# Optimization experiments

Measured on AMD Instinct MI355X. Metric: run time of the kernel, lower is better.

## Reference

```python
import jax, jax.numpy as jnp
import numpy as np

N, E, FE = 20000, 160000, 500000
IN, HC, HEADS = 128, 64, 4
HEADC = HC // HEADS          # 16
DV = HEADC                   # 16
KHOP = 3
NUM_T = 128
OUT = 1
CST = 1e-5


def _lin(key, fan_in, fan_out):
    kw, kb = jax.random.split(key)
    s = 1.0 / np.sqrt(fan_in)
    W = jax.random.uniform(kw, (fan_in, fan_out), minval=-s, maxval=s, dtype=jnp.float32)
    b = jax.random.uniform(kb, (fan_out,), minval=-s, maxval=s, dtype=jnp.float32)
    return W, b


def setup_inputs() -> dict:
    key = jax.random.key(0)
    ks = jax.random.split(key, 16)
    x = jax.random.normal(ks[0], (N, IN), dtype=jnp.float32)
    edge_index = jax.random.randint(ks[1], (2, E), 0, N, dtype=jnp.int32)
    full_edge_index = jax.random.randint(ks[2], (2, FE), 0, N, dtype=jnp.int32)
    time_steps = jax.random.randint(ks[3], (N,), 0, NUM_T, dtype=jnp.int32)
    Wi, bi = _lin(ks[4], IN, HC)
    Wt1, bt1 = _lin(ks[5], HC, 4 * HC)
    Wt2, bt2 = _lin(ks[6], 4 * HC, HC)
    WQ, bQ = _lin(ks[7], HC, HEADS * HEADC)
    WK, bK = _lin(ks[8], HC, HEADS * HEADC)
    WV, bV = _lin(ks[9], HC, HEADS * DV)
    Wo, bo = _lin(ks[10], HEADS * DV, DV)
    hopwise = jnp.ones((KHOP + 1,), dtype=jnp.float32)
    headwise = jnp.zeros((HEADS, KHOP), dtype=jnp.float32)
    Wf1, bf1 = _lin(ks[11], 2 * DV, DV)
    Wf2, bf2 = _lin(ks[12], DV, OUT)
    return dict(x=x, edge_index=edge_index, full_edge_index=full_edge_index,
                time_steps=time_steps, Wi=Wi, bi=bi, Wt1=Wt1, bt1=bt1,
                Wt2=Wt2, bt2=bt2, WQ=WQ, bQ=bQ, WK=WK, bK=bK, WV=WV, bV=bV,
                Wo=Wo, bo=bo, hopwise=hopwise, headwise=headwise,
                Wf1=Wf1, bf1=bf1, Wf2=Wf2, bf2=bf2)


def _sin_emb(t, dim, num_steps, rescale=4000.0):
    # Sinusoidal timestep embedding rescaled by num_steps (diffusion style).
    t = t.astype(jnp.float32) * (rescale / num_steps)
    half = dim // 2
    freqs = jnp.exp(-jnp.log(10000.0) / (half - 1) * jnp.arange(half, dtype=jnp.float32))
    args = t[:, None] * freqs[None, :]
    return jnp.concatenate([jnp.sin(args), jnp.cos(args)], axis=-1)


def reference(x, edge_index, full_edge_index, time_steps,
              Wi, bi, Wt1, bt1, Wt2, bt2, WQ, bQ, WK, bK, WV, bV,
              Wo, bo, hopwise, headwise, Wf1, bf1, Wf2, bf2):
    n = x.shape[0]
    row, col = edge_index[0], edge_index[1]

    # random-walk norm: deg over destination (col), norm gathered at source (row)
    deg = jax.ops.segment_sum(jnp.ones_like(col, dtype=x.dtype), col, num_segments=n)
    deg_inv = jnp.where(deg > 0, 1.0 / deg, 0.0)
    norm = deg_inv[row]                                   # [E]

    t_emb = _sin_emb(time_steps, HC, NUM_T)               # [N, HC]
    t_emb = jax.nn.silu(t_emb @ Wt1 + bt1) @ Wt2 + bt2    # [N, HC]

    h = jax.nn.relu(x @ Wi + bi + t_emb)                  # [N, HC]

    Q = (1.0 + jax.nn.elu(h @ WQ + bQ)).reshape(n, HEADS, HEADC)
    Kf = (1.0 + jax.nn.elu(h @ WK + bK)).reshape(n, HEADS, HEADC)
    V = (h @ WV + bV).reshape(n, HEADS, DV)

    M = jnp.einsum('nhi,nhj->nhij', Kf, V)                # [N, H, hc, dv]
    hidden = V * hopwise[0]
    layerwise = jax.nn.softmax(headwise, axis=0)          # softmax over heads

    for hop in range(KHOP):
        # gather-scale-scatter message passing (random walk propagation)
        M = jax.ops.segment_sum(M[row] * norm[:, None, None, None], col, num_segments=n)
        Kf = jax.ops.segment_sum(Kf[row] * norm[:, None, None], col, num_segments=n)
        H = jnp.einsum('nhi,nhij->nhj', Q, M)             # [N, H, dv]
        C = jnp.einsum('nhi,nhi->nh', Q, Kf)[..., None] + CST
        gamma = hopwise[hop + 1] * layerwise[:, hop][:, None]   # [H, 1]
        hidden = hidden + gamma * (H / C)

    # multi_concat output projection
    hidden = hidden.reshape(n, HEADS * DV) @ Wo + bo      # [N, DV]

    src, dst = full_edge_index[0], full_edge_index[1]
    he = jnp.concatenate([hidden[src], hidden[dst]], axis=-1)  # [FE, 2*DV]
    edge_logits = jax.nn.silu(he @ Wf1 + bf1) @ Wf2 + bf2      # [FE, OUT]
    return edge_logits, hidden
```

## Files before the change

kernel.cpp:

```cpp
#include <hip/hip_runtime.h>
#include <math.h>


#define HC 64
#define HEADS 4
#define KHOP 3
#define NUM_T 128
#define MSZ 1024
#define SLOTS 64
#define CST 1e-5f

typedef float f32x2 __attribute__((ext_vector_type(2)));

__device__ __forceinline__ float bf2f(unsigned short s) { return __uint_as_float(((unsigned int)s) << 16); }
__device__ __forceinline__ float bfu_lo(unsigned int u) { return __uint_as_float(u << 16); }
__device__ __forceinline__ float bfu_hi(unsigned int u) { return __uint_as_float(u & 0xffff0000u); }
__device__ __forceinline__ unsigned short f2bf(float f) {
    unsigned int u = __float_as_uint(f);
    u = (u + 0x7fffu + ((u >> 16) & 1u)) >> 16;
    return (unsigned short)u;
}
__device__ __forceinline__ unsigned int pack4fp8(float a, float b, float c, float d) {
    int r = __builtin_amdgcn_cvt_pk_fp8_f32(a, b, 0, false);
    r = __builtin_amdgcn_cvt_pk_fp8_f32(c, d, r, true);
    return (unsigned int)r;
}

__global__ void k_fill(const int* __restrict__ row, const int* __restrict__ col,
                       int* __restrict__ cnt, int* __restrict__ csr, int E) {
    int e = blockIdx.x * 256 + threadIdx.x;
    if (e >= E) return;
    int c = col[e];
    int r = row[e];
    int k = atomicAdd(&cnt[c], 1);
    if (k < SLOTS) csr[c * SLOTS + k] = r;
}

__global__ __launch_bounds__(256) void k_misc(
    const float* __restrict__ Wt1, const float* __restrict__ bt1,
    const float* __restrict__ Wt2, const float* __restrict__ bt2,
    const float* __restrict__ hopwise, const float* __restrict__ headwise,
    const int* __restrict__ cnt,
    float* __restrict__ gamma, float* __restrict__ table,
    float* __restrict__ inv_deg, int n) {
    if (blockIdx.x >= 32) {
        int i = (blockIdx.x - 32) * 256 + threadIdx.x;
        if (i < n) {
            int d = cnt[i];
            inv_deg[i] = (d > 0) ? 1.0f / (float)min(d, SLOTS) : 0.0f;
        }
        return;
    }
    if (blockIdx.x == 0 && threadIdx.x == 0) {
        for (int k = 0; k < KHOP; k++) {
            float m = -1e30f;
            for (int h2 = 0; h2 < HEADS; h2++) m = fmaxf(m, headwise[h2 * KHOP + k]);
            float ex[HEADS]; float s = 0.f;
            for (int h2 = 0; h2 < HEADS; h2++) { ex[h2] = expf(headwise[h2 * KHOP + k] - m); s += ex[h2]; }
            for (int h2 = 0; h2 < HEADS; h2++) gamma[k * HEADS + h2] = hopwise[k + 1] * ex[h2] / s;
        }
    }
    int slot = threadIdx.x >> 6;
    int j = threadIdx.x & 63;
    int tval = blockIdx.x * 4 + slot;
    __shared__ float emb_s[4][64];
    __shared__ float z1_s[4][256];
    {
        float t = (float)tval * 31.25f;
        float e;
        if (j < 32) e = sinf(t * expf(-0.2971077539347156f * (float)j));
        else        e = cosf(t * expf(-0.2971077539347156f * (float)(j - 32)));
        emb_s[slot][j] = e;
    }
    __syncthreads();
    {
        #pragma unroll
        for (int k = 0; k < 4; k++) {
            int o = j + 64 * k;
            float acc = bt1[o];
            for (int i = 0; i < 64; i++) acc += emb_s[slot][i] * Wt1[i * 256 + o];
            z1_s[slot][o] = acc / (1.f + expf(-acc));
        }
    }
    __syncthreads();
    {
        float acc = bt2[j];
        for (int i = 0; i < 256; i++) acc += z1_s[slot][i] * Wt2[i * 64 + j];
        table[tval * 64 + j] = acc;
    }
}

__global__ __launch_bounds__(256) void k_node(
    const float* __restrict__ x, const int* __restrict__ time_steps,
    const float* __restrict__ temb, const float* __restrict__ Wi,
    const float* __restrict__ bi,
    const float* __restrict__ WQ, const float* __restrict__ bQ,
    const float* __restrict__ WK, const float* __restrict__ bK,
    const float* __restrict__ WV, const float* __restrict__ bV,
    const float* __restrict__ hopwise, const float* __restrict__ inv_deg,
    float* __restrict__ Q, unsigned short* __restrict__ Kf0,
    unsigned short* __restrict__ Vbuf, float* __restrict__ hidden, int n) {
    __shared__ float xs[16][128];
    __shared__ float hs[16][64];
    int j = threadIdx.x & 63;
    int slot = threadIdx.x >> 6;
    int nbase = blockIdx.x * 16;
    int nvalid = min(16, n - nbase);
    const float4* xg = (const float4*)(x + (size_t)nbase * 128);
    float4* xs4 = (float4*)&xs[0][0];
    for (int idx = threadIdx.x; idx < nvalid * 32; idx += 256) xs4[idx] = xg[idx];
    __syncthreads();
    int nl = slot * 4;
    {
        float acc[4];
        #pragma unroll
        for (int k = 0; k < 4; k++) acc[k] = 0.f;
        #pragma unroll 8
        for (int i = 0; i < 128; i++) {
            float w = Wi[i * 64 + j];
            #pragma unroll
            for (int k = 0; k < 4; k++) acc[k] += xs[nl + k][i] * w;
        }
        float bj = bi[j];
        #pragma unroll
        for (int k = 0; k < 4; k++) {
            int node = nbase + nl + k;
            float te = (node < n) ? temb[time_steps[node] * 64 + j] : 0.f;
            hs[nl + k][j] = fmaxf(acc[k] + bj + te, 0.f);
        }
    }
    __syncthreads();
    float aq[4], ak[4], av[4];
    #pragma unroll
    for (int k = 0; k < 4; k++) { aq[k] = bQ[j]; ak[k] = bK[j]; av[k] = bV[j]; }
    #pragma unroll 4
    for (int i = 0; i < 64; i++) {
        float wq = WQ[i * 64 + j], wk = WK[i * 64 + j], wv = WV[i * 64 + j];
        #pragma unroll
        for (int k = 0; k < 4; k++) {
            float hv = hs[nl + k][i];
            aq[k] += hv * wq; ak[k] += hv * wk; av[k] += hv * wv;
        }
    }
    float h0 = hopwise[0];
    #pragma unroll
    for (int k = 0; k < 4; k++) {
        int node = nbase + nl + k;
        if (node < n) {
            float q  = 1.f + ((aq[k] > 0.f) ? aq[k] : (expf(aq[k]) - 1.f));
            float kf = 1.f + ((ak[k] > 0.f) ? ak[k] : (expf(ak[k]) - 1.f));
            float inv = inv_deg[node];
            Q[(size_t)node * 64 + j] = q;
            Kf0[(size_t)node * 64 + j] = f2bf(kf * inv);
            Vbuf[(size_t)node * 64 + j] = f2bf(av[k]);
            hidden[(size_t)node * 64 + j] = av[k] * h0;
        }
    }
}

template<int MODE>
__global__ __launch_bounds__(256) void k_hop(
    const unsigned char* __restrict__ Mold, const unsigned short* __restrict__ Kfold,
    const unsigned short* __restrict__ Vbuf,
    const int* __restrict__ cnt, const int* __restrict__ csr,
    const float* __restrict__ inv_deg, const float* __restrict__ Q,
    const float* __restrict__ gamma,
    unsigned char* __restrict__ Mnew, unsigned short* __restrict__ Kfnew,
    float* __restrict__ hidden, int hop, int write_out,
    const float* __restrict__ Wo, const float* __restrict__ bo,
    const float* __restrict__ Wf1, float* __restrict__ out16,
    float* __restrict__ Pbuf, int n) {
    constexpr int DEPTH = (MODE == 0) ? 4 : 8;
    int lane = threadIdx.x & 63;
    int node = blockIdx.x * 4 + (threadIdx.x >> 6);
    if (node >= n) return;
    int grp = lane >> 4;
    int deg = min(cnt[node], SLOTS);
    int degU = __builtin_amdgcn_readfirstlane(deg);
    int sidx = csr[(size_t)node * SLOTS + lane];
    float qv = Q[(size_t)node * 64 + lane];
    float acc[16];
    #pragma unroll
    for (int t = 0; t < 16; t++) acc[t] = 0.f;
    float kacc = 0.f;

    for (int base = 0; base < degU; base += DEPTH) {
        unsigned short kraw[DEPTH];
        uint4 m0[DEPTH], m1[DEPTH];
        #pragma unroll
        for (int t = 0; t < DEPTH; t++) {
            int d = base + t;
            int dc = (d < degU) ? d : (degU - 1);
            int s = __builtin_amdgcn_readlane(sidx, dc);
            kraw[t] = Kfold[(size_t)s * 64 + lane];
            if constexpr (MODE == 0) {
                const uint4* vp = (const uint4*)((const unsigned char*)Vbuf + (size_t)s * 128 + grp * 32);
                m0[t] = vp[0];
                m1[t] = vp[1];
            } else {
                m0[t] = *(const uint4*)(Mold + (size_t)s * MSZ + lane * 16);
            }
        }
        #pragma unroll
        for (int t = 0; t < DEPTH; t++) {
            float wt = (base + t < degU) ? 1.f : 0.f;
            float kf = bf2f(kraw[t]);
            kacc = fmaf(wt, kf, kacc);
            if constexpr (MODE == 0) {
                float kw = kf * wt;
                acc[0]  = fmaf(kw, bfu_lo(m0[t].x), acc[0]);
                acc[1]  = fmaf(kw, bfu_hi(m0[t].x), acc[1]);
                acc[2]  = fmaf(kw, bfu_lo(m0[t].y), acc[2]);
                acc[3]  = fmaf(kw, bfu_hi(m0[t].y), acc[3]);
                acc[4]  = fmaf(kw, bfu_lo(m0[t].z), acc[4]);
                acc[5]  = fmaf(kw, bfu_hi(m0[t].z), acc[5]);
                acc[6]  = fmaf(kw, bfu_lo(m0[t].w), acc[6]);
                acc[7]  = fmaf(kw, bfu_hi(m0[t].w), acc[7]);
                acc[8]  = fmaf(kw, bfu_lo(m1[t].x), acc[8]);
                acc[9]  = fmaf(kw, bfu_hi(m1[t].x), acc[9]);
                acc[10] = fmaf(kw, bfu_lo(m1[t].y), acc[10]);
                acc[11] = fmaf(kw, bfu_hi(m1[t].y), acc[11]);
                acc[12] = fmaf(kw, bfu_lo(m1[t].z), acc[12]);
                acc[13] = fmaf(kw, bfu_hi(m1[t].z), acc[13]);
                acc[14] = fmaf(kw, bfu_lo(m1[t].w), acc[14]);
                acc[15] = fmaf(kw, bfu_hi(m1[t].w), acc[15]);
            } else {
                f32x2 p;
                p = __builtin_amdgcn_cvt_pk_f32_fp8((int)m0[t].x, false); acc[0]  = fmaf(wt, p.x, acc[0]);  acc[1]  = fmaf(wt, p.y, acc[1]);
                p = __builtin_amdgcn_cvt_pk_f32_fp8((int)m0[t].x, true);  acc[2]  = fmaf(wt, p.x, acc[2]);  acc[3]  = fmaf(wt, p.y, acc[3]);
                p = __builtin_amdgcn_cvt_pk_f32_fp8((int)m0[t].y, false); acc[4]  = fmaf(wt, p.x, acc[4]);  acc[5]  = fmaf(wt, p.y, acc[5]);
                p = __builtin_amdgcn_cvt_pk_f32_fp8((int)m0[t].y, true);  acc[6]  = fmaf(wt, p.x, acc[6]);  acc[7]  = fmaf(wt, p.y, acc[7]);
                p = __builtin_amdgcn_cvt_pk_f32_fp8((int)m0[t].z, false); acc[8]  = fmaf(wt, p.x, acc[8]);  acc[9]  = fmaf(wt, p.y, acc[9]);
                p = __builtin_amdgcn_cvt_pk_f32_fp8((int)m0[t].z, true);  acc[10] = fmaf(wt, p.x, acc[10]); acc[11] = fmaf(wt, p.y, acc[11]);
                p = __builtin_amdgcn_cvt_pk_f32_fp8((int)m0[t].w, false); acc[12] = fmaf(wt, p.x, acc[12]); acc[13] = fmaf(wt, p.y, acc[13]);
                p = __builtin_amdgcn_cvt_pk_f32_fp8((int)m0[t].w, true);  acc[14] = fmaf(wt, p.x, acc[14]); acc[15] = fmaf(wt, p.y, acc[15]);
            }
        }
    }

    if (write_out) {
        float inv = inv_deg[node];
        uint4 st;
        st.x = pack4fp8(acc[0] * inv,  acc[1] * inv,  acc[2] * inv,  acc[3] * inv);
        st.y = pack4fp8(acc[4] * inv,  acc[5] * inv,  acc[6] * inv,  acc[7] * inv);
        st.z = pack4fp8(acc[8] * inv,  acc[9] * inv,  acc[10] * inv, acc[11] * inv);
        st.w = pack4fp8(acc[12] * inv, acc[13] * inv, acc[14] * inv, acc[15] * inv);
        *(uint4*)(Mnew + (size_t)node * MSZ + lane * 16) = st;
        Kfnew[(size_t)node * 64 + lane] = f2bf(kacc * inv);
    }

    float c = qv * kacc;
    c += __shfl_xor(c, 1); c += __shfl_xor(c, 2); c += __shfl_xor(c, 4); c += __shfl_xor(c, 8);

    float w0[16];
    #pragma unroll
    for (int t = 0; t < 16; t++) w0[t] = qv * acc[t];
    float w1r[8];
    #pragma unroll
    for (int t = 0; t < 8; t++) {
        float a = w0[2 * t], b = w0[2 * t + 1];
        float mine = (lane & 1) ? b : a, th = (lane & 1) ? a : b;
        w1r[t] = mine + __shfl_xor(th, 1);
    }
    float w2r[4];
    #pragma unroll
    for (int t = 0; t < 4; t++) {
        float a = w1r[2 * t], b = w1r[2 * t + 1];
        float mine = (lane & 2) ? b : a, th = (lane & 2) ? a : b;
        w2r[t] = mine + __shfl_xor(th, 2);
    }
    float w3r[2];
    #pragma unroll
    for (int t = 0; t < 2; t++) {
        float a = w2r[2 * t], b = w2r[2 * t + 1];
        float mine = (lane & 4) ? b : a, th = (lane & 4) ? a : b;
        w3r[t] = mine + __shfl_xor(th, 4);
    }
    float Hv;
    {
        float a = w3r[0], b = w3r[1];
        float mine = (lane & 8) ? b : a, th = (lane & 8) ? a : b;
        Hv = mine + __shfl_xor(th, 8);
    }

    float g = gamma[hop * HEADS + grp];
    float contrib = g * Hv / (c + CST);
    size_t hoff = (size_t)node * 64 + lane;
    if (write_out) {
        hidden[hoff] = hidden[hoff] + contrib;
    } else {
        float hid = hidden[hoff] + contrib;
        const float4* wop = (const float4*)(Wo + lane * 16);
        float4 wo0 = wop[0], wo1 = wop[1], wo2 = wop[2], wo3 = wop[3];
        float v[16];
        v[0] = hid * wo0.x;  v[1] = hid * wo0.y;  v[2] = hid * wo0.z;  v[3] = hid * wo0.w;
        v[4] = hid * wo1.x;  v[5] = hid * wo1.y;  v[6] = hid * wo1.z;  v[7] = hid * wo1.w;
        v[8] = hid * wo2.x;  v[9] = hid * wo2.y;  v[10] = hid * wo2.z; v[11] = hid * wo2.w;
        v[12] = hid * wo3.x; v[13] = hid * wo3.y; v[14] = hid * wo3.z; v[15] = hid * wo3.w;
        #pragma unroll
        for (int m = 32; m >= 1; m >>= 1) {
            #pragma unroll
            for (int o = 0; o < 16; o++) v[o] += __shfl_xor(v[o], m);
        }
        #pragma unroll
        for (int o = 0; o < 16; o++) v[o] += bo[o];
        if (lane == 0) {
            float4* op = (float4*)(out16 + (size_t)node * 16);
            op[0] = make_float4(v[0],  v[1],  v[2],  v[3]);
            op[1] = make_float4(v[4],  v[5],  v[6],  v[7]);
            op[2] = make_float4(v[8],  v[9],  v[10], v[11]);
            op[3] = make_float4(v[12], v[13], v[14], v[15]);
        }
        if (lane < 32) {
            int o = lane & 15, half = lane >> 4;
            const float* wf = Wf1 + (size_t)(half * 16) * 16 + o;
            float p = 0.f;
            #pragma unroll
            for (int i = 0; i < 16; i++) p += v[i] * wf[i * 16];
            Pbuf[(size_t)node * 32 + lane] = p;
        }
    }
}

__global__ __launch_bounds__(256) void k_edge(
    const int* __restrict__ src, const int* __restrict__ dst,
    const float* __restrict__ Pbuf,
    const float* __restrict__ bf1, const float* __restrict__ Wf2,
    const float* __restrict__ bf2,
    float* __restrict__ out, int fe) {
    __shared__ float b1[16];
    __shared__ float w2[16];
    __shared__ float b2s;
    int t = threadIdx.x;
    if (t < 16) { b1[t] = bf1[t]; w2[t] = Wf2[t]; }
    if (t == 0) b2s = bf2[0];
    __syncthreads();
    int e = blockIdx.x * 256 + t;
    if (e >= fe) return;
    int s = src[e], d = dst[e];
    const float4* p1 = (const float4*)(Pbuf + (size_t)s * 32);
    const float4* p2 = (const float4*)(Pbuf + (size_t)d * 32 + 16);
    float z[16];
    #pragma unroll
    for (int q = 0; q < 4; q++) {
        float4 a = p1[q]; float4 b = p2[q];
        z[q * 4 + 0] = a.x + b.x; z[q * 4 + 1] = a.y + b.y;
        z[q * 4 + 2] = a.z + b.z; z[q * 4 + 3] = a.w + b.w;
    }
    float acc = b2s;
    #pragma unroll
    for (int o = 0; o < 16; o++) {
        float zz = z[o] + b1[o];
        zz = zz / (1.f + expf(-zz));
        acc += zz * w2[o];
    }
    out[e] = acc;
}

extern "C" void kernel_launch(void* const* d_in, const int* in_sizes, int n_in,
                              void* d_out, int out_size, void* d_ws, size_t ws_size,
                              hipStream_t stream) {
    const float* x        = (const float*)d_in[0];
    const int*   eidx     = (const int*)d_in[1];
    const int*   feidx    = (const int*)d_in[2];
    const int*   tsteps   = (const int*)d_in[3];
    const float* Wi  = (const float*)d_in[4];
    const float* bi  = (const float*)d_in[5];
    const float* Wt1 = (const float*)d_in[6];
    const float* bt1 = (const float*)d_in[7];
    const float* Wt2 = (const float*)d_in[8];
    const float* bt2 = (const float*)d_in[9];
    const float* WQ  = (const float*)d_in[10];
    const float* bQ  = (const float*)d_in[11];
    const float* WK  = (const float*)d_in[12];
    const float* bK  = (const float*)d_in[13];
    const float* WV  = (const float*)d_in[14];
    const float* bV  = (const float*)d_in[15];
    const float* Wo  = (const float*)d_in[16];
    const float* bo  = (const float*)d_in[17];
    const float* hopwise  = (const float*)d_in[18];
    const float* headwise = (const float*)d_in[19];
    const float* Wf1 = (const float*)d_in[20];
    const float* bf1 = (const float*)d_in[21];
    const float* Wf2 = (const float*)d_in[22];
    const float* bf2 = (const float*)d_in[23];

    const int N  = in_sizes[3];
    const int E  = in_sizes[1] / 2;
    const int FE = in_sizes[2] / 2;
    const int* row = eidx;
    const int* col = eidx + E;
    const int* fsrc = feidx;
    const int* fdst = feidx + FE;

    char* ws = (char*)d_ws;
    size_t off = 0;
    auto alloc = [&](size_t bytes) -> char* {
        char* p = ws + off;
        off = (off + bytes + 255) & ~(size_t)255;
        return p;
    };
    float* gamma     = (float*)alloc(KHOP * HEADS * sizeof(float));
    int*   cnt       = (int*)alloc((size_t)N * 4);
    int*   csr       = (int*)alloc((size_t)N * SLOTS * 4);
    float* inv_deg   = (float*)alloc((size_t)N * 4);
    float* temb      = (float*)alloc((size_t)NUM_T * HC * 4);
    float* Qbuf      = (float*)alloc((size_t)N * HC * 4);
    unsigned short* Kf0  = (unsigned short*)alloc((size_t)N * HC * 2);
    unsigned short* Kf_a = (unsigned short*)alloc((size_t)N * HC * 2);
    unsigned short* Kf_b = (unsigned short*)alloc((size_t)N * HC * 2);
    unsigned short* Vbuf = (unsigned short*)alloc((size_t)N * HC * 2);
    float* hidden    = (float*)alloc((size_t)N * HC * 4);
    unsigned char* M_a = (unsigned char*)alloc((size_t)N * MSZ);
    unsigned char* M_b = (unsigned char*)alloc((size_t)N * MSZ);
    float* Pbuf      = (float*)alloc((size_t)N * 32 * 4);
    (void)ws_size;

    float* out_edges = (float*)d_out;
    float* out_hid16 = (float*)d_out + FE;

    const int miscBlocks = 32 + (N + 255) / 256;
    const int hopBlocks = (N + 3) / 4;

    (void)hipMemsetAsync(cnt, 0, (size_t)N * 4, stream);
    k_fill<<<(E + 255) / 256, 256, 0, stream>>>(row, col, cnt, csr, E);
    k_misc<<<miscBlocks, 256, 0, stream>>>(Wt1, bt1, Wt2, bt2, hopwise, headwise,
                                           cnt, gamma, temb, inv_deg, N);
    k_node<<<(N + 15) / 16, 256, 0, stream>>>(x, tsteps, temb, Wi, bi,
                                              WQ, bQ, WK, bK, WV, bV, hopwise, inv_deg,
                                              Qbuf, Kf0, Vbuf, hidden, N);
    k_hop<0><<<hopBlocks, 256, 0, stream>>>(nullptr, Kf0, Vbuf, cnt, csr, inv_deg, Qbuf, gamma,
                                            M_a, Kf_a, hidden, 0, 1, Wo, bo, Wf1, out_hid16, Pbuf, N);
    k_hop<1><<<hopBlocks, 256, 0, stream>>>(M_a, Kf_a, nullptr, cnt, csr, inv_deg, Qbuf, gamma,
                                            M_b, Kf_b, hidden, 1, 1, Wo, bo, Wf1, out_hid16, Pbuf, N);
    k_hop<1><<<hopBlocks, 256, 0, stream>>>(M_b, Kf_b, nullptr, cnt, csr, inv_deg, Qbuf, gamma,
                                            M_a, Kf_a, hidden, 2, 0, Wo, bo, Wf1, out_hid16, Pbuf, N);
    k_edge<<<(FE + 255) / 256, 256, 0, stream>>>(fsrc, fdst, Pbuf, bf1, Wf2, bf2,
                                                 out_edges, FE);
}
```

Baseline: 270.3 us.

## Split hop loop into full-depth and tail, shrink hop blocks, widen timestep MLP

```diff
diff --git a/kernel.cpp b/kernel.cpp
--- a/kernel.cpp
+++ b/kernel.cpp
@@ -43,8 +43,8 @@
     const int* __restrict__ cnt,
     float* __restrict__ gamma, float* __restrict__ table,
     float* __restrict__ inv_deg, int n) {
-    if (blockIdx.x >= 32) {
-        int i = (blockIdx.x - 32) * 256 + threadIdx.x;
+    if (blockIdx.x >= NUM_T) {
+        int i = (blockIdx.x - NUM_T) * 256 + threadIdx.x;
         if (i < n) {
             int d = cnt[i];
             inv_deg[i] = (d > 0) ? 1.0f / (float)min(d, SLOTS) : 0.0f;
@@ -60,34 +60,36 @@
             for (int h2 = 0; h2 < HEADS; h2++) gamma[k * HEADS + h2] = hopwise[k + 1] * ex[h2] / s;
         }
     }
-    int slot = threadIdx.x >> 6;
-    int j = threadIdx.x & 63;
-    int tval = blockIdx.x * 4 + slot;
-    __shared__ float emb_s[4][64];
-    __shared__ float z1_s[4][256];
+    int t = threadIdx.x;
+    int tval = blockIdx.x;
+    __shared__ float emb_s[64];
+    __shared__ float z1_s[256];
+    __shared__ float ps_s[4][64];
+    if (t < 64) {
+        float tt = (float)tval * 31.25f;
+        float e;
+        if (t < 32) e = sinf(tt * expf(-0.2971077539347156f * (float)t));
+        else        e = cosf(tt * expf(-0.2971077539347156f * (float)(t - 32)));
+        emb_s[t] = e;
+    }
+    __syncthreads();
     {
-        float t = (float)tval * 31.25f;
-        float e;
-        if (j < 32) e = sinf(t * expf(-0.2971077539347156f * (float)j));
-        else        e = cosf(t * expf(-0.2971077539347156f * (float)(j - 32)));
-        emb_s[slot][j] = e;
+        float acc = bt1[t];
+        #pragma unroll 8
+        for (int i = 0; i < 64; i++) acc += emb_s[i] * Wt1[i * 256 + t];
+        z1_s[t] = acc / (1.f + expf(-acc));
     }
     __syncthreads();
     {
-        #pragma unroll
-        for (int k = 0; k < 4; k++) {
-            int o = j + 64 * k;
-            float acc = bt1[o];
-            for (int i = 0; i < 64; i++) acc += emb_s[slot][i] * Wt1[i * 256 + o];
-            z1_s[slot][o] = acc / (1.f + expf(-acc));
-        }
-    }
-    __syncthreads();
-    {
-        float acc = bt2[j];
-        for (int i = 0; i < 256; i++) acc += z1_s[slot][i] * Wt2[i * 64 + j];
-        table[tval * 64 + j] = acc;
-    }
+        int j = t & 63, p = t >> 6;
+        float acc = 0.f;
+        #pragma unroll 8
+        for (int i = 0; i < 64; i++) acc += z1_s[p * 64 + i] * Wt2[(p * 64 + i) * 64 + j];
+        ps_s[p][j] = acc;
+    }
+    __syncthreads();
+    if (t < 64)
+        table[tval * 64 + t] = ps_s[0][t] + ps_s[1][t] + ps_s[2][t] + ps_s[3][t] + bt2[t];
 }
 
 __global__ __launch_bounds__(256) void k_node(
@@ -159,7 +161,7 @@
 }
 
 template<int MODE>
-__global__ __launch_bounds__(256) void k_hop(
+__global__ __launch_bounds__(128) void k_hop(
     const unsigned char* __restrict__ Mold, const unsigned short* __restrict__ Kfold,
     const unsigned short* __restrict__ Vbuf,
     const int* __restrict__ cnt, const int* __restrict__ csr,
@@ -172,68 +174,119 @@
     float* __restrict__ Pbuf, int n) {
     constexpr int DEPTH = (MODE == 0) ? 4 : 8;
     int lane = threadIdx.x & 63;
-    int node = blockIdx.x * 4 + (threadIdx.x >> 6);
+    int node = blockIdx.x * 2 + (threadIdx.x >> 6);
     if (node >= n) return;
     int grp = lane >> 4;
     int deg = min(cnt[node], SLOTS);
-    int degU = __builtin_amdgcn_readfirstlane(deg);
     int sidx = csr[(size_t)node * SLOTS + lane];
     float qv = Q[(size_t)node * 64 + lane];
+    size_t hoff = (size_t)node * 64 + lane;
+    float hid_in = hidden[hoff];
+    int degU = __builtin_amdgcn_readfirstlane(deg);
     float acc[16];
     #pragma unroll
     for (int t = 0; t < 16; t++) acc[t] = 0.f;
     float kacc = 0.f;
 
-    for (int base = 0; base < degU; base += DEPTH) {
+    int d = 0;
+    for (; d + DEPTH <= degU; d += DEPTH) {
         unsigned short kraw[DEPTH];
         uint4 m0[DEPTH], m1[DEPTH];
         #pragma unroll
         for (int t = 0; t < DEPTH; t++) {
-            int d = base + t;
-            int dc = (d < degU) ? d : (degU - 1);
-            int s = __builtin_amdgcn_readlane(sidx, dc);
+            int s = __builtin_amdgcn_readlane(sidx, d + t);
             kraw[t] = Kfold[(size_t)s * 64 + lane];
             if constexpr (MODE == 0) {
                 const uint4* vp = (const uint4*)((const unsigned char*)Vbuf + (size_t)s * 128 + grp * 32);
-                m0[t] = vp[0];
-                m1[t] = vp[1];
+                m0[t] = vp[0]; m1[t] = vp[1];
             } else {
                 m0[t] = *(const uint4*)(Mold + (size_t)s * MSZ + lane * 16);
             }
         }
         #pragma unroll
         for (int t = 0; t < DEPTH; t++) {
-            float wt = (base + t < degU) ? 1.f : 0.f;
             float kf = bf2f(kraw[t]);
-            kacc = fmaf(wt, kf, kacc);
+            kacc += kf;
             if constexpr (MODE == 0) {
-                float kw = kf * wt;
-                acc[0]  = fmaf(kw, bfu_lo(m0[t].x), acc[0]);
-                acc[1]  = fmaf(kw, bfu_hi(m0[t].x), acc[1]);
-                acc[2]  = fmaf(kw, bfu_lo(m0[t].y), acc[2]);
-                acc[3]  = fmaf(kw, bfu_hi(m0[t].y), acc[3]);
-                acc[4]  = fmaf(kw, bfu_lo(m0[t].z), acc[4]);
-                acc[5]  = fmaf(kw, bfu_hi(m0[t].z), acc[5]);
-                acc[6]  = fmaf(kw, bfu_lo(m0[t].w), acc[6]);
-                acc[7]  = fmaf(kw, bfu_hi(m0[t].w), acc[7]);
-                acc[8]  = fmaf(kw, bfu_lo(m1[t].x), acc[8]);
-                acc[9]  = fmaf(kw, bfu_hi(m1[t].x), acc[9]);
-                acc[10] = fmaf(kw, bfu_lo(m1[t].y), acc[10]);
-                acc[11] = fmaf(kw, bfu_hi(m1[t].y), acc[11]);
-                acc[12] = fmaf(kw, bfu_lo(m1[t].z), acc[12]);
-                acc[13] = fmaf(kw, bfu_hi(m1[t].z), acc[13]);
-                acc[14] = fmaf(kw, bfu_lo(m1[t].w), acc[14]);
-                acc[15] = fmaf(kw, bfu_hi(m1[t].w), acc[15]);
+                acc[0]  = fmaf(kf, bfu_lo(m0[t].x), acc[0]);
+                acc[1]  = fmaf(kf, bfu_hi(m0[t].x), acc[1]);
+                acc[2]  = fmaf(kf, bfu_lo(m0[t].y), acc[2]);
+                acc[3]  = fmaf(kf, bfu_hi(m0[t].y), acc[3]);
+                acc[4]  = fmaf(kf, bfu_lo(m0[t].z), acc[4]);
+                acc[5]  = fmaf(kf, bfu_hi(m0[t].z), acc[5]);
+                acc[6]  = fmaf(kf, bfu_lo(m0[t].w), acc[6]);
+                acc[7]  = fmaf(kf, bfu_hi(m0[t].w), acc[7]);
+                acc[8]  = fmaf(kf, bfu_lo(m1[t].x), acc[8]);
+                acc[9]  = fmaf(kf, bfu_hi(m1[t].x), acc[9]);
+                acc[10] = fmaf(kf, bfu_lo(m1[t].y), acc[10]);
+                acc[11] = fmaf(kf, bfu_hi(m1[t].y), acc[11]);
+                acc[12] = fmaf(kf, bfu_lo(m1[t].z), acc[12]);
+                acc[13] = fmaf(kf, bfu_hi(m1[t].z), acc[13]);
+                acc[14] = fmaf(kf, bfu_lo(m1[t].w), acc[14]);
+                acc[15] = fmaf(kf, bfu_hi(m1[t].w), acc[15]);
             } else {
                 f32x2 p;
-                p = __builtin_amdgcn_cvt_pk_f32_fp8((int)m0[t].x, false); acc[0]  = fmaf(wt, p.x, acc[0]);  acc[1]  = fmaf(wt, p.y, acc[1]);
-                p = __builtin_amdgcn_cvt_pk_f32_fp8((int)m0[t].x, true);  acc[2]  = fmaf(wt, p.x, acc[2]);  acc[3]  = fmaf(wt, p.y, acc[3]);
-                p = __builtin_amdgcn_cvt_pk_f32_fp8((int)m0[t].y, false); acc[4]  = fmaf(wt, p.x, acc[4]);  acc[5]  = fmaf(wt, p.y, acc[5]);
-                p = __builtin_amdgcn_cvt_pk_f32_fp8((int)m0[t].y, true);  acc[6]  = fmaf(wt, p.x, acc[6]);  acc[7]  = fmaf(wt, p.y, acc[7]);
-                p = __builtin_amdgcn_cvt_pk_f32_fp8((int)m0[t].z, false); acc[8]  = fmaf(wt, p.x, acc[8]);  acc[9]  = fmaf(wt, p.y, acc[9]);
-                p = __builtin_amdgcn_cvt_pk_f32_fp8((int)m0[t].z, true);  acc[10] = fmaf(wt, p.x, acc[10]); acc[11] = fmaf(wt, p.y, acc[11]);
-                p = __builtin_amdgcn_cvt_pk_f32_fp8((int)m0[t].w, false); acc[12] = fmaf(wt, p.x, acc[12]); acc[13] = fmaf(wt, p.y, acc[13]);
-                p = __builtin_amdgcn_cvt_pk_f32_fp8((int)m0[t].w, true);  acc[14] = fmaf(wt, p.x, acc[14]); acc[15] = fmaf(wt, p.y, acc[15]);
+                p = __builtin_amdgcn_cvt_pk_f32_fp8((int)m0[t].x, false); acc[0]  += p.x; acc[1]  += p.y;
+                p = __builtin_amdgcn_cvt_pk_f32_fp8((int)m0[t].x, true);  acc[2]  += p.x; acc[3]  += p.y;
+                p = __builtin_amdgcn_cvt_pk_f32_fp8((int)m0[t].y, false); acc[4]  += p.x; acc[5]  += p.y;
+                p = __builtin_amdgcn_cvt_pk_f32_fp8((int)m0[t].y, true);  acc[6]  += p.x; acc[7]  += p.y;
+                p = __builtin_amdgcn_cvt_pk_f32_fp8((int)m0[t].z, false); acc[8]  += p.x; acc[9]  += p.y;
+                p = __builtin_amdgcn_cvt_pk_f32_fp8((int)m0[t].z, true);  acc[10] += p.x; acc[11] += p.y;
+                p = __builtin_amdgcn_cvt_pk_f32_fp8((int)m0[t].w, false); acc[12] += p.x; acc[13] += p.y;
+                p = __builtin_amdgcn_cvt_pk_f32_fp8((int)m0[t].w, true);  acc[14] += p.x; acc[15] += p.y;
+            }
+        }
+    }
+    if (d < degU) {
+        int rem = degU - d;
+        unsigned short kraw[DEPTH];
+        uint4 m0[DEPTH], m1[DEPTH];
+        #pragma unroll
+        for (int t = 0; t < DEPTH - 1; t++) {
+            if (t < rem) {
+                int s = __builtin_amdgcn_readlane(sidx, d + t);
+                kraw[t] = Kfold[(size_t)s * 64 + lane];
+                if constexpr (MODE == 0) {
+                    const uint4* vp = (const uint4*)((const unsigned char*)Vbuf + (size_t)s * 128 + grp * 32);
+                    m0[t] = vp[0]; m1[t] = vp[1];
+                } else {
+                    m0[t] = *(const uint4*)(Mold + (size_t)s * MSZ + lane * 16);
+                }
+            }
+        }
+        #pragma unroll
+        for (int t = 0; t < DEPTH - 1; t++) {
+            if (t < rem) {
+                float kf = bf2f(kraw[t]);
+                kacc += kf;
+                if constexpr (MODE == 0) {
+                    acc[0]  = fmaf(kf, bfu_lo(m0[t].x), acc[0]);
+                    acc[1]  = fmaf(kf, bfu_hi(m0[t].x), acc[1]);
+                    acc[2]  = fmaf(kf, bfu_lo(m0[t].y), acc[2]);
+                    acc[3]  = fmaf(kf, bfu_hi(m0[t].y), acc[3]);
+                    acc[4]  = fmaf(kf, bfu_lo(m0[t].z), acc[4]);
+                    acc[5]  = fmaf(kf, bfu_hi(m0[t].z), acc[5]);
+                    acc[6]  = fmaf(kf, bfu_lo(m0[t].w), acc[6]);
+                    acc[7]  = fmaf(kf, bfu_hi(m0[t].w), acc[7]);
+                    acc[8]  = fmaf(kf, bfu_lo(m1[t].x), acc[8]);
+                    acc[9]  = fmaf(kf, bfu_hi(m1[t].x), acc[9]);
+                    acc[10] = fmaf(kf, bfu_lo(m1[t].y), acc[10]);
+                    acc[11] = fmaf(kf, bfu_hi(m1[t].y), acc[11]);
+                    acc[12] = fmaf(kf, bfu_lo(m1[t].z), acc[12]);
+                    acc[13] = fmaf(kf, bfu_hi(m1[t].z), acc[13]);
+                    acc[14] = fmaf(kf, bfu_lo(m1[t].w), acc[14]);
+                    acc[15] = fmaf(kf, bfu_hi(m1[t].w), acc[15]);
+                } else {
+                    f32x2 p;
+                    p = __builtin_amdgcn_cvt_pk_f32_fp8((int)m0[t].x, false); acc[0]  += p.x; acc[1]  += p.y;
+                    p = __builtin_amdgcn_cvt_pk_f32_fp8((int)m0[t].x, true);  acc[2]  += p.x; acc[3]  += p.y;
+                    p = __builtin_amdgcn_cvt_pk_f32_fp8((int)m0[t].y, false); acc[4]  += p.x; acc[5]  += p.y;
+                    p = __builtin_amdgcn_cvt_pk_f32_fp8((int)m0[t].y, true);  acc[6]  += p.x; acc[7]  += p.y;
+                    p = __builtin_amdgcn_cvt_pk_f32_fp8((int)m0[t].z, false); acc[8]  += p.x; acc[9]  += p.y;
+                    p = __builtin_amdgcn_cvt_pk_f32_fp8((int)m0[t].z, true);  acc[10] += p.x; acc[11] += p.y;
+                    p = __builtin_amdgcn_cvt_pk_f32_fp8((int)m0[t].w, false); acc[12] += p.x; acc[13] += p.y;
+                    p = __builtin_amdgcn_cvt_pk_f32_fp8((int)m0[t].w, true);  acc[14] += p.x; acc[15] += p.y;
+                }
             }
         }
     }
@@ -285,11 +338,10 @@
 
     float g = gamma[hop * HEADS + grp];
     float contrib = g * Hv / (c + CST);
-    size_t hoff = (size_t)node * 64 + lane;
     if (write_out) {
-        hidden[hoff] = hidden[hoff] + contrib;
+        hidden[hoff] = hid_in + contrib;
     } else {
-        float hid = hidden[hoff] + contrib;
+        float hid = hid_in + contrib;
         const float4* wop = (const float4*)(Wo + lane * 16);
         float4 wo0 = wop[0], wo1 = wop[1], wo2 = wop[2], wo3 = wop[3];
         float v[16];
@@ -419,8 +471,8 @@
     float* out_edges = (float*)d_out;
     float* out_hid16 = (float*)d_out + FE;
 
-    const int miscBlocks = 32 + (N + 255) / 256;
-    const int hopBlocks = (N + 3) / 4;
+    const int miscBlocks = NUM_T + (N + 255) / 256;
+    const int hopBlocks = (N + 1) / 2;
 
     (void)hipMemsetAsync(cnt, 0, (size_t)N * 4, stream);
     k_fill<<<(E + 255) / 256, 256, 0, stream>>>(row, col, cnt, csr, E);
@@ -429,11 +481,11 @@
     k_node<<<(N + 15) / 16, 256, 0, stream>>>(x, tsteps, temb, Wi, bi,
                                               WQ, bQ, WK, bK, WV, bV, hopwise, inv_deg,
                                               Qbuf, Kf0, Vbuf, hidden, N);
-    k_hop<0><<<hopBlocks, 256, 0, stream>>>(nullptr, Kf0, Vbuf, cnt, csr, inv_deg, Qbuf, gamma,
+    k_hop<0><<<hopBlocks, 128, 0, stream>>>(nullptr, Kf0, Vbuf, cnt, csr, inv_deg, Qbuf, gamma,
                                             M_a, Kf_a, hidden, 0, 1, Wo, bo, Wf1, out_hid16, Pbuf, N);
-    k_hop<1><<<hopBlocks, 256, 0, stream>>>(M_a, Kf_a, nullptr, cnt, csr, inv_deg, Qbuf, gamma,
+    k_hop<1><<<hopBlocks, 128, 0, stream>>>(M_a, Kf_a, nullptr, cnt, csr, inv_deg, Qbuf, gamma,
                                             M_b, Kf_b, hidden, 1, 1, Wo, bo, Wf1, out_hid16, Pbuf, N);
-    k_hop<1><<<hopBlocks, 256, 0, stream>>>(M_b, Kf_b, nullptr, cnt, csr, inv_deg, Qbuf, gamma,
+    k_hop<1><<<hopBlocks, 128, 0, stream>>>(M_b, Kf_b, nullptr, cnt, csr, inv_deg, Qbuf, gamma,
                                             M_a, Kf_a, hidden, 2, 0, Wo, bo, Wf1, out_hid16, Pbuf, N);
     k_edge<<<(FE + 255) / 256, 256, 0, stream>>>(fsrc, fdst, Pbuf, bf1, Wf2, bf2,
                                                  out_edges, FE);
```

New measurement: 253.9 us. 1.06x faster.
